# Optimization experiments

Measured on AMD Instinct MI355X. Metric: run time of the kernel, lower is better.

## Reference

```python
import jax, jax.numpy as jnp
import numpy as np

NQ, NT, NA = 10000, 50000, 50000
E_GR, E_LT, E_SIM, E_COMP, E_GEN = 50000, 50000, 80000, 100000, 50000
HID, NH, HC, DOT, NL = 512, 4, 128, 256, 2
NEG_SLOPE = 0.2  # PyG GATv2Conv default negative_slope


def _gatv2(x_src, x_dst, src, dst, Wl, bl, Wr, br, att, bias, n_dst):
    # GATv2: x_j = lin_l(x_src), x_i = lin_r(x_dst); e = att . leaky_relu(x_i + x_j)
    xl = (x_src @ Wl + bl).reshape(-1, NH, HC)   # [Ns,H,C]
    xr = (x_dst @ Wr + br).reshape(-1, NH, HC)   # [Nd,H,C]
    m = jax.nn.leaky_relu(xl[src] + xr[dst], NEG_SLOPE)      # [E,H,C]
    logits = jnp.einsum('ehc,hc->eh', m, att)                # [E,H]
    lmax = jax.lax.stop_gradient(jax.ops.segment_max(logits, dst, num_segments=n_dst))
    lmax = jnp.where(jnp.isfinite(lmax), lmax, 0.0)
    ex = jnp.exp(logits - lmax[dst])
    denom = jax.ops.segment_sum(ex, dst, num_segments=n_dst)
    alpha = ex / (denom[dst] + 1e-16)                        # softmax over incoming edges
    out = jax.ops.segment_sum(xl[src] * alpha[:, :, None], dst, num_segments=n_dst)
    return out.reshape(n_dst, NH * HC) + bias


def _layernorm(x, g, b):
    mu = x.mean(-1, keepdims=True)
    var = ((x - mu) ** 2).mean(-1, keepdims=True)
    return (x - mu) / jnp.sqrt(var + 1e-5) * g + b


def _forward(xq, xt, xa, answer_features,
             qp_W, qp_b, tp_W, tp_b, ap_W, ap_b,
             afp_W1, afp_b1, afp_W2, afp_b2,
             conv_Wl, conv_bl, conv_Wr, conv_br, conv_att, conv_bias,
             qh_W, qh_b, qh_g, qh_beta, rh_W, rh_b, rh_g, rh_beta, score_bias,
             ei_gr, ei_lt, ei_sim, ei_comp, ei_gen):
    hq = xq @ qp_W + qp_b
    ht = xt @ tp_W + tp_b
    ha = xa @ ap_W + ap_b
    # add_self_loops=True only for ('query','similar_to','query')
    loops = jnp.arange(NQ, dtype=ei_sim.dtype)
    sim_src = jnp.concatenate([ei_sim[0], loops])
    sim_dst = jnp.concatenate([ei_sim[1], loops])
    for l in range(NL):
        P = lambda r: (conv_Wl[l, r], conv_bl[l, r], conv_Wr[l, r], conv_br[l, r], conv_att[l, r], conv_bias[l, r])
        o_gr = _gatv2(hq, ht, ei_gr[0], ei_gr[1], *P(0), NT)          # query -> think
        o_rgr = _gatv2(ht, hq, ei_gr[1], ei_gr[0], *P(1), NQ)         # think -> query (rev)
        o_lt = _gatv2(ht, ha, ei_lt[0], ei_lt[1], *P(2), NA)          # think -> answer
        o_rlt = _gatv2(ha, ht, ei_lt[1], ei_lt[0], *P(3), NT)         # answer -> think (rev)
        o_sim = _gatv2(hq, hq, sim_src, sim_dst, *P(4), NQ)           # query -> query
        o_cmp = _gatv2(ht, ht, ei_comp[0], ei_comp[1], *P(5), NT)     # think -> think
        # HeteroConv aggr='mean' across relations per destination type, then relu
        hq = jax.nn.relu((o_rgr + o_sim) / 2.0)
        ht = jax.nn.relu((o_gr + o_rlt + o_cmp) / 3.0)
        ha = jax.nn.relu(o_lt)
    q_emb = hq[ei_gen[0]]
    a_emb = ha[ei_gen[1]]
    t_emb = ht[ei_gen[1]]  # faithful to source: think indexed with answer-side index
    af_emb = jax.nn.relu(answer_features @ afp_W1 + afp_b1) @ afp_W2 + afp_b2
    q = _layernorm(q_emb @ qh_W + qh_b, qh_g, qh_beta)
    r = _layernorm(jnp.concatenate([t_emb, a_emb, af_emb], -1) @ rh_W + rh_b, rh_g, rh_beta)
    return (q * r).sum(-1) / jnp.sqrt(jnp.float32(DOT)) + score_bias


def setup_inputs() -> dict:
    ks = jax.random.split(jax.random.key(0), 40)
    n = lambda j, shape, s=0.05: jax.random.normal(ks[j], shape, jnp.float32) * s
    ri = lambda j, shape, hi: jax.random.randint(ks[j], shape, 0, hi, jnp.int32)
    return dict(
        xq=n(0, (NQ, 384), 1.0), xt=n(1, (NT, 384), 1.0), xa=n(2, (NA, 384), 1.0),
        answer_features=n(3, (E_GEN, 6), 1.0),
        qp_W=n(4, (384, HID)), qp_b=n(5, (HID,)),
        tp_W=n(6, (384, HID)), tp_b=n(7, (HID,)),
        ap_W=n(8, (384, HID)), ap_b=n(9, (HID,)),
        afp_W1=n(10, (6, 64)), afp_b1=n(11, (64,)),
        afp_W2=n(12, (64, HID)), afp_b2=n(13, (HID,)),
        conv_Wl=n(14, (NL, 6, HID, HID)), conv_bl=n(15, (NL, 6, HID)),
        conv_Wr=n(16, (NL, 6, HID, HID)), conv_br=n(17, (NL, 6, HID)),
        conv_att=n(18, (NL, 6, NH, HC)), conv_bias=n(19, (NL, 6, HID)),
        qh_W=n(20, (HID, DOT)), qh_b=n(21, (DOT,)),
        qh_g=jnp.ones((DOT,), jnp.float32), qh_beta=jnp.zeros((DOT,), jnp.float32),
        rh_W=n(22, (HID * 3, DOT)), rh_b=n(23, (DOT,)),
        rh_g=jnp.ones((DOT,), jnp.float32), rh_beta=jnp.zeros((DOT,), jnp.float32),
        score_bias=jnp.zeros((1,), jnp.float32),
        ei_gr=jnp.stack([ri(24, (E_GR,), NQ), ri(25, (E_GR,), NT)]),
        ei_lt=jnp.stack([ri(26, (E_LT,), NT), ri(27, (E_LT,), NA)]),
        ei_sim=ri(28, (2, E_SIM), NQ),
        ei_comp=ri(29, (2, E_COMP), NT),
        ei_gen=jnp.stack([ri(30, (E_GEN,), NQ), ri(31, (E_GEN,), NA)]),
    )


def reference(xq, xt, xa, answer_features,
              qp_W, qp_b, tp_W, tp_b, ap_W, ap_b,
              afp_W1, afp_b1, afp_W2, afp_b2,
              conv_Wl, conv_bl, conv_Wr, conv_br, conv_att, conv_bias,
              qh_W, qh_b, qh_g, qh_beta, rh_W, rh_b, rh_g, rh_beta, score_bias,
              ei_gr, ei_lt, ei_sim, ei_comp, ei_gen):
    return _forward(xq, xt, xa, answer_features,
                    qp_W, qp_b, tp_W, tp_b, ap_W, ap_b,
                    afp_W1, afp_b1, afp_W2, afp_b2,
                    conv_Wl, conv_bl, conv_Wr, conv_br, conv_att, conv_bias,
                    qh_W, qh_b, qh_g, qh_beta, rh_W, rh_b, rh_g, rh_beta, score_bias,
                    ei_gr, ei_lt, ei_sim, ei_comp, ei_gen)
```

## Files before the change

### kernel.cpp

```cpp
#include <hip/hip_runtime.h>
#include <cstdio>
#include <type_traits>

#define NQ 10000
#define NT 50000
#define NA 50000
#define E_GR 50000
#define E_LT 50000
#define E_SIM 80000
#define E_COMP 100000
#define E_GEN 50000
#define NEG_SLOPE 0.2f

#define NDTOT 220000
#define NSTOT 220000
#define ETOT  390000
__device__ __constant__ const int c_degOff[7]  = {0, 50000, 60000, 110000, 120000, 170000, 220000};
__device__ __constant__ const int c_sOff[7]    = {0, 10000, 60000, 110000, 120000, 170000, 220000};
__device__ __constant__ const int c_eOff[7]    = {0, 50000, 100000, 150000, 240000, 340000, 390000};
__device__ __constant__ const int c_nb[6]      = {49, 10, 49, 10, 49, 49};
__device__ __constant__ const int c_nbOff[7]   = {0, 49, 59, 108, 118, 167, 216};
__device__ __constant__ const int c_snb[6]     = {10, 49, 49, 10, 49, 49};
__device__ __constant__ const int c_snbOff[7]  = {0, 10, 59, 108, 118, 167, 216};

typedef unsigned short bf16_t;
typedef unsigned int u32;
typedef __attribute__((ext_vector_type(8))) short short8v;
typedef __attribute__((ext_vector_type(4))) float f32x4;

__device__ __forceinline__ float bf2f(u32 bits) { return __uint_as_float(bits << 16); }
__device__ __forceinline__ u32 f2bf(float f) {
  u32 u = __float_as_uint(f);
  return (u + 0x7FFFu + ((u >> 16) & 1u)) >> 16;
}
__device__ __forceinline__ u32 pack2(float a, float b) { return f2bf(a) | (f2bf(b) << 16); }
__device__ __forceinline__ void unpack8(uint4 u, float* f) {
  f[0] = bf2f(u.x & 0xffffu); f[1] = bf2f(u.x >> 16);
  f[2] = bf2f(u.y & 0xffffu); f[3] = bf2f(u.y >> 16);
  f[4] = bf2f(u.z & 0xffffu); f[5] = bf2f(u.z >> 16);
  f[6] = bf2f(u.w & 0xffffu); f[7] = bf2f(u.w >> 16);
}

__device__ __forceinline__ void gload16(const void* g, void* l) {
  __builtin_amdgcn_global_load_lds(
      (const __attribute__((address_space(1))) void*)g,
      (__attribute__((address_space(3))) void*)l, 16, 0, 0);
}

template <typename CT>
__global__ __launch_bounds__(512, 4) void bgemm(
    const bf16_t* __restrict__ A0, const bf16_t* __restrict__ Bt0,
    const float* __restrict__ bias0, CT* __restrict__ C0,
    const int* __restrict__ ridx0, int N0, const int* __restrict__ Nc0,
    const bf16_t* __restrict__ A1, const bf16_t* __restrict__ Bt1,
    const float* __restrict__ bias1, CT* __restrict__ C1,
    const int* __restrict__ ridx1, int N1, const int* __restrict__ Nc1,
    int K, int M, int accumulate)
{
  __shared__ short lds[3][12288];
  const int z = blockIdx.z;
  const bf16_t* A   = z ? A1 : A0;
  const bf16_t* Bt  = z ? Bt1 : Bt0;
  const float* bias = z ? bias1 : bias0;
  CT* C             = z ? C1 : C0;
  const int* ridx   = z ? ridx1 : ridx0;
  const int* Nc     = z ? Nc1 : Nc0;
  int N             = z ? N1 : N0;
  if (Nc) N = *Nc;

  const int tid = threadIdx.x;
  const int ncol = gridDim.x;
  const int nband = (N + 127) >> 7;
  int lin = blockIdx.y * ncol + blockIdx.x;
  if (lin >= ncol * nband) return;

  int band, col;
  const int full = (nband >> 3) * 8 * ncol;
  if (lin < full) {
    int g = lin >> 3, x = lin & 7;
    band = x + 8 * (g / ncol);
    col  = g % ncol;
  } else {
    int r = lin - full;
    band = (nband & ~7) + r / ncol;
    col  = r % ncol;
  }
  const int bm = band * 128, bn = col * 256;

  const int lane = tid & 63;
  const int w = tid >> 6;
  const int wr = w >> 2, wc = w & 3;
  const int fr = lane & 15, fg = lane >> 4;

  const int kg = (((tid & 3) ^ ((tid >> 3) & 3)) << 3);
  const int rr = tid >> 2;
  int ra = min(bm + rr, N - 1);
  const bf16_t* gA0 = A + (size_t)(ridx ? ridx[ra] : ra) * K + kg;
  const bf16_t* gB0 = Bt + (size_t)(bn + rr) * K + kg;
  const bf16_t* gB1 = Bt + (size_t)(bn + 128 + rr) * K + kg;
  const int wb = w << 9;

  f32x4 acc[4][4];
#pragma unroll
  for (int i = 0; i < 4; ++i)
#pragma unroll
    for (int j = 0; j < 4; ++j) acc[i][j] = (f32x4){0.f, 0.f, 0.f, 0.f};

  auto stage = [&](int buf, int k0) {
    short* base = &lds[buf][0];
    gload16(gA0 + k0, base + wb);
    gload16(gB0 + k0, base + 4096 + wb);
    gload16(gB1 + k0, base + 8192 + wb);
  };

  const int nsteps = K >> 5;
  stage(0, 0);
  const int co = (fg ^ ((fr >> 1) & 3)) << 3;
  for (int s = 0; s < nsteps; ++s) {
    const int cur = s % 3;
    if (s + 1 < nsteps) {
      stage((s + 1) % 3, (s + 1) << 5);
      asm volatile("s_waitcnt vmcnt(3)" ::: "memory");
    } else {
      asm volatile("s_waitcnt vmcnt(0)" ::: "memory");
    }
    __builtin_amdgcn_s_barrier();
    asm volatile("" ::: "memory");
    const short* LA = &lds[cur][0];
    const short* LB = &lds[cur][4096];
    short8v b[4];
#pragma unroll
    for (int j = 0; j < 4; ++j) {
      int R = wc * 64 + j * 16 + fr;
      b[j] = *(const short8v*)&LB[R * 32 + co];
    }
#pragma unroll
    for (int i = 0; i < 4; ++i) {
      int R = wr * 64 + i * 16 + fr;
      short8v a = *(const short8v*)&LA[R * 32 + co];
#pragma unroll
      for (int j = 0; j < 4; ++j)
        acc[i][j] = __builtin_amdgcn_mfma_f32_16x16x32_bf16(b[j], a,
                                                            acc[i][j], 0, 0, 0);
    }
    asm volatile("" ::: "memory");
  }

  float4 bv[4];
#pragma unroll
  for (int j = 0; j < 4; ++j) {
    bv[j] = make_float4(0.f, 0.f, 0.f, 0.f);
    if (!accumulate && bias)
      bv[j] = *(const float4*)(bias + bn + wc * 64 + j * 16 + fg * 4);
  }
#pragma unroll
  for (int i = 0; i < 4; ++i) {
    const int n = bm + wr * 64 + i * 16 + fr;
    if (n >= N) continue;
#pragma unroll
    for (int j = 0; j < 4; ++j) {
      const int m0 = bn + wc * 64 + j * 16 + fg * 4;
      f32x4 v = acc[i][j];
      if constexpr (std::is_same<CT, float>::value) {
        float* p = C + (size_t)n * M + m0;
        if (accumulate) {
          float4 o = *(float4*)p;
          o.x += v[0]; o.y += v[1]; o.z += v[2]; o.w += v[3];
          *(float4*)p = o;
        } else {
          *(float4*)p = make_float4(v[0] + bv[j].x, v[1] + bv[j].y,
                                    v[2] + bv[j].z, v[3] + bv[j].w);
        }
      } else {
        uint2 o;
        o.x = pack2(v[0] + bv[j].x, v[1] + bv[j].y);
        o.y = pack2(v[2] + bv[j].z, v[3] + bv[j].w);
        *(uint2*)(C + (size_t)n * M + m0) = o;
      }
    }
  }
}

__device__ __forceinline__ void wT_tile(
    const float* __restrict__ W, bf16_t* __restrict__ Wt, int K, int M)
{
  __shared__ float sm[32][33];
  int mb = blockIdx.x * 32, kb = blockIdx.y * 32;
  int tx = threadIdx.x & 31, ty = threadIdx.x >> 5;
#pragma unroll
  for (int i = 0; i < 4; ++i)
    sm[ty + i * 8][tx] = W[(size_t)(kb + ty + i * 8) * M + mb + tx];
  __syncthreads();
#pragma unroll
  for (int i = 0; i < 4; ++i)
    Wt[(size_t)(mb + ty + i * 8) * K + kb + tx] = (bf16_t)f2bf(sm[tx][ty + i * 8]);
}

__global__ __launch_bounds__(256) void convert_wT(
    const float* __restrict__ W, bf16_t* __restrict__ Wt, int K, int M)
{
  wT_tile(W + (size_t)blockIdx.z * K * M, Wt + (size_t)blockIdx.z * K * M, K, M);
}
__global__ __launch_bounds__(256) void convert_wT24(
    const float* __restrict__ Wl, bf16_t* __restrict__ wl,
    const float* __restrict__ Wr, bf16_t* __restrict__ wr)
{
  int z = blockIdx.z;
  size_t o = (size_t)(z < 12 ? z : z - 12) * 512 * 512;
  if (z < 12) wT_tile(Wl + o, wl + o, 512, 512);
  else        wT_tile(Wr + o, wr + o, 512, 512);
}
__global__ __launch_bounds__(256) void convert_wT3(
    const float* __restrict__ W0, const float* __restrict__ W1,
    const float* __restrict__ W2, bf16_t* __restrict__ T0,
    bf16_t* __restrict__ T1, bf16_t* __restrict__ T2)
{
  int z = blockIdx.z;
  const float* W = z == 0 ? W0 : z == 1 ? W1 : W2;
  bf16_t* T = z == 0 ? T0 : z == 1 ? T1 : T2;
  wT_tile(W, T, 384, 512);
}
__global__ __launch_bounds__(256) void convert_wT4h(
    const float* __restrict__ qh, const float* __restrict__ rh,
    bf16_t* __restrict__ wqh, bf16_t* __restrict__ wrh)
{
  int z = blockIdx.z;
  if (z == 0) wT_tile(qh, wqh, 512, 256);
  else        wT_tile(rh + (size_t)(z - 1) * 512 * 256,
                      wrh + (size_t)(z - 1) * 256 * 512, 512, 256);
}

#define N4_XQ (NQ * 96)
#define N4_XT (NT * 96)
#define N4_XA (NA * 96)
__global__ __launch_bounds__(256) void cast3(
    const float* __restrict__ xq, const float* __restrict__ xt,
    const float* __restrict__ xa, bf16_t* __restrict__ xqb,
    bf16_t* __restrict__ xtb, bf16_t* __restrict__ xab)
{
  long g = (long)blockIdx.x * 256 + threadIdx.x;
  const float* in; bf16_t* out; long idx;
  if (g < N4_XQ)                { in = xq; out = xqb; idx = g; }
  else if (g < N4_XQ + N4_XT)   { in = xt; out = xtb; idx = g - N4_XQ; }
  else if (g < N4_XQ + N4_XT + N4_XA) { in = xa; out = xab; idx = g - N4_XQ - N4_XT; }
  else return;
  float4 v = ((const float4*)in)[idx];
  uint2 o;
  o.x = pack2(v.x, v.y);
  o.y = pack2(v.z, v.w);
  ((uint2*)out)[idx] = o;
}

__global__ __launch_bounds__(256) void combine_bias6(
    const float* __restrict__ cb, float* __restrict__ bcAll)
{
  int g = blockIdx.x * 256 + threadIdx.x;
  if (g >= 6 * 512) return;
  int row = g >> 9, j = g & 511;
  int l = row / 3, kind = row % 3;
  const float* b = cb + (size_t)l * 6 * 512;
  float v;
  if (kind == 0)      v = (b[0 * 512 + j] + b[3 * 512 + j] + b[5 * 512 + j]) / 3.f;
  else if (kind == 1) v = (b[1 * 512 + j] + b[4 * 512 + j]) * 0.5f;
  else                v = b[2 * 512 + j];
  bcAll[(size_t)row * 512 + j] = v;
}

__device__ __forceinline__ int find_rel6(int g, const int* off) {
  int r = 0;
#pragma unroll
  for (int k = 1; k < 6; ++k) r += (g >= off[k]);
  return r;
}

__global__ __launch_bounds__(256) void hist6(
    const int* __restrict__ d0, const int* __restrict__ d1,
    const int* __restrict__ d2, const int* __restrict__ d3,
    const int* __restrict__ d4, const int* __restrict__ d5,
    const int* __restrict__ s0p, const int* __restrict__ s1p,
    const int* __restrict__ s2p, const int* __restrict__ s3p,
    const int* __restrict__ s4p, const int* __restrict__ s5p,
    int* __restrict__ degAll, int* __restrict__ sdegAll, int* __restrict__ pos)
{
  int g = blockIdx.x * 256 + threadIdx.x;
  if (g >= ETOT) return;
  int r = find_rel6(g, c_eOff);
  int le = g - c_eOff[r];
  const int* dp = r == 0 ? d0 : r == 1 ? d1 : r == 2 ? d2 : r == 3 ? d3
                : r == 4 ? d4 : d5;
  const int* sp = r == 0 ? s0p : r == 1 ? s1p : r == 2 ? s2p : r == 3 ? s3p
                : r == 4 ? s4p : s5p;
  pos[g] = atomicAdd(&degAll[c_degOff[r] + dp[le]], 1);
  atomicAdd(&sdegAll[c_sOff[r] + sp[le]], 1);
}

template <int PRED, int SRC>
__global__ __launch_bounds__(256) void scan1_6(
    const int* __restrict__ in, int* __restrict__ out, int* __restrict__ bsum)
{
  __shared__ int sm[256];
  int b = blockIdx.x;
  const int* nbOff = SRC ? c_snbOff : c_nbOff;
  const int* dOff  = SRC ? c_sOff : c_degOff;
  int r = 0;
#pragma unroll
  for (int k = 1; k < 6; ++k) r += (b >= nbOff[k]);
  int lb = b - nbOff[r];
  int base0 = dOff[r], n = dOff[r + 1] - base0;
  int t = threadIdx.x;
  int base = lb * 1024 + t * 4;
  int v[4], sum = 0;
#pragma unroll
  for (int k = 0; k < 4; ++k) {
    int raw = (base + k < n) ? in[base0 + base + k] : 0;
    v[k] = PRED == 0 ? raw : PRED == 1 ? (raw >= 2 ? 1 : 0) : (raw >= 1 ? 1 : 0);
    sum += v[k];
  }
  sm[t] = sum;
  __syncthreads();
  for (int off = 1; off < 256; off <<= 1) {
    int x = (t >= off) ? sm[t - off] : 0;
    __syncthreads();
    sm[t] += x;
    __syncthreads();
  }
  int run = (t > 0) ? sm[t - 1] : 0;
  if (t == 255) bsum[r * 64 + lb] = sm[255];
#pragma unroll
  for (int k = 0; k < 4; ++k) {
    if (base + k < n) out[base0 + base + k] = run;
    run += v[k];
  }
}

template <int SRC>
__global__ __launch_bounds__(64) void scan2_6(
    int* __restrict__ bsum, int* __restrict__ total)
{
  __shared__ int sm[64];
  int r = blockIdx.x;
  int nb = SRC ? c_snb[r] : c_nb[r];
  int t = threadIdx.x;
  int v = (t < nb) ? bsum[r * 64 + t] : 0;
  sm[t] = v;
  __syncthreads();
  for (int off = 1; off < 64; off <<= 1) {
    int x = (t >= off) ? sm[t - off] : 0;
    __syncthreads();
    sm[t] += x;
    __syncthreads();
  }
  if (t < nb) bsum[r * 64 + t] = sm[t] - v;
  if (total && t == nb - 1) total[r] = sm[t];
}

template <int SRC>
__global__ __launch_bounds__(256) void scan3_6(
    int* __restrict__ out, const int* __restrict__ bsum)
{
  int g = blockIdx.x * 256 + threadIdx.x;
  if (g >= (SRC ? NSTOT : NDTOT)) return;
  const int* dOff = SRC ? c_sOff : c_degOff;
  int r = find_rel6(g, dOff);
  int ln = g - dOff[r];
  out[g] += bsum[r * 64 + (ln >> 10)];
}

__global__ __launch_bounds__(256) void scatter6(
    const int* __restrict__ d0, const int* __restrict__ d1,
    const int* __restrict__ d2, const int* __restrict__ d3,
    const int* __restrict__ d4, const int* __restrict__ d5,
    const int* __restrict__ s0p, const int* __restrict__ s1p,
    const int* __restrict__ s2p, const int* __restrict__ s3p,
    const int* __restrict__ s4p, const int* __restrict__ s5p,
    const int* __restrict__ startAll, const int* __restrict__ pos,
    const int* __restrict__ sposAll,
    int* __restrict__ eidxAll, int* __restrict__ srcCAll)
{
  int g = blockIdx.x * 256 + threadIdx.x;
  if (g >= ETOT) return;
  int r = find_rel6(g, c_eOff);
  int le = g - c_eOff[r];
  const int* dp = r == 0 ? d0 : r == 1 ? d1 : r == 2 ? d2 : r == 3 ? d3
                : r == 4 ? d4 : d5;
  const int* sp = r == 0 ? s0p : r == 1 ? s1p : r == 2 ? s2p : r == 3 ? s3p
                : r == 4 ? s4p : s5p;
  eidxAll[c_eOff[r] + startAll[c_degOff[r] + dp[le]] + pos[g]] = le;
  srcCAll[g] = sposAll[c_sOff[r] + sp[le]];
}

template <int SRC, int THR>
__global__ __launch_bounds__(256) void compact6(
    const int* __restrict__ degA, const int* __restrict__ cposA,
    int* __restrict__ cidxA)
{
  int g = blockIdx.x * 256 + threadIdx.x;
  if (g >= (SRC ? NSTOT : NDTOT)) return;
  if (degA[g] >= THR) {
    const int* dOff = SRC ? c_sOff : c_degOff;
    int r = find_rel6(g, dOff);
    cidxA[dOff[r] + cposA[g]] = g - dOff[r];
  }
}

__global__ __launch_bounds__(256) void gat_fused(
    const bf16_t* __restrict__ xl, const bf16_t* __restrict__ xr,
    const int* __restrict__ srcC, const int* __restrict__ start,
    const int* __restrict__ deg, const int* __restrict__ eidx,
    const int* __restrict__ cpos, const float* __restrict__ att,
    bf16_t* __restrict__ acc, int Nd, int accumulate,
    const float* __restrict__ bc, float inv_div)
{
  int d = blockIdx.x * 4 + (threadIdx.x >> 6);
  if (d >= Nd) return;
  int lane = threadIdx.x & 63;

  float acc8[8] = {0.f, 0.f, 0.f, 0.f, 0.f, 0.f, 0.f, 0.f};
  int n = deg[d], s0 = start[d];
  if (n == 1) {
    int s = srcC[eidx[s0]];
    unpack8(*(const uint4*)(xl + (size_t)s * 512 + lane * 8), acc8);
  } else if (n > 1) {
    float xrr[8];
    unpack8(*(const uint4*)(xr + (size_t)cpos[d] * 512 + lane * 8), xrr);
    float at[8];
    *(float4*)(at)     = *(const float4*)(att + lane * 8);
    *(float4*)(at + 4) = *(const float4*)(att + lane * 8 + 4);
    float den = 0.f;
    int sN = srcC[eidx[s0]];
    for (int i = 0; i < n; ++i) {
      int s = sN;
      if (i + 1 < n) sN = srcC[eidx[s0 + i + 1]];
      float f[8];
      unpack8(*(const uint4*)(xl + (size_t)s * 512 + lane * 8), f);
      float p = 0.f;
#pragma unroll
      for (int k = 0; k < 8; ++k) {
        float x = f[k] + xrr[k];
        p = fmaf(at[k], x >= 0.f ? x : NEG_SLOPE * x, p);
      }
#pragma unroll
      for (int m = 8; m >= 1; m >>= 1) p += __shfl_xor(p, m);
      float ex = __expf(p);
      den += ex;
#pragma unroll
      for (int k = 0; k < 8; ++k) acc8[k] = fmaf(ex, f[k], acc8[k]);
    }
    float inv = 1.f / (den + 1e-16f);
#pragma unroll
    for (int k = 0; k < 8; ++k) acc8[k] *= inv;
  }

  bf16_t* out = acc + (size_t)d * 512 + lane * 8;
  if (accumulate) {
    float old[8];
    unpack8(*(const uint4*)out, old);
#pragma unroll
    for (int k = 0; k < 8; ++k) acc8[k] += old[k];
  }
  if (bc) {
    float bcv[8];
    *(float4*)(bcv)     = *(const float4*)(bc + lane * 8);
    *(float4*)(bcv + 4) = *(const float4*)(bc + lane * 8 + 4);
#pragma unroll
    for (int k = 0; k < 8; ++k)
      acc8[k] = fmaxf(fmaf(acc8[k], inv_div, bcv[k]), 0.f);
  }
  uint4 s;
  s.x = pack2(acc8[0], acc8[1]); s.y = pack2(acc8[2], acc8[3]);
  s.z = pack2(acc8[4], acc8[5]); s.w = pack2(acc8[6], acc8[7]);
  *(uint4*)out = s;
}

__global__ __launch_bounds__(256) void af_hidden(
    const float* __restrict__ af, const float* __restrict__ W1,
    const float* __restrict__ b1, bf16_t* __restrict__ out, int n)
{
  int t = blockIdx.x * blockDim.x + threadIdx.x;
  if (t >= n * 64) return;
  int i = t >> 6, j = t & 63;
  const float* a = af + (size_t)i * 6;
  float s = b1[j];
#pragma unroll
  for (int k = 0; k < 6; ++k) s = fmaf(a[k], W1[k * 64 + j], s);
  out[t] = (bf16_t)f2bf(fmaxf(s, 0.f));
}

__global__ __launch_bounds__(256) void build_sim(
    const int* __restrict__ ei, int* __restrict__ ss, int* __restrict__ sd)
{
  int t = blockIdx.x * blockDim.x + threadIdx.x;
  if (t >= E_SIM + NQ) return;
  if (t < E_SIM) { ss[t] = ei[t]; sd[t] = ei[E_SIM + t]; }
  else           { ss[t] = t - E_SIM; sd[t] = t - E_SIM; }
}

__global__ __launch_bounds__(256) void head_final(
    const float* __restrict__ qpre, const float* __restrict__ rpre,
    const float* __restrict__ qg, const float* __restrict__ qb,
    const float* __restrict__ rg, const float* __restrict__ rb,
    const float* __restrict__ score_bias, float* __restrict__ out, int E)
{
  int e = blockIdx.x * 4 + (threadIdx.x >> 6);
  if (e >= E) return;
  int lane = threadIdx.x & 63;

  float4 q = *(const float4*)(qpre + (size_t)e * 256 + lane * 4);
  float s = q.x + q.y + q.z + q.w;
#pragma unroll
  for (int m = 32; m >= 1; m >>= 1) s += __shfl_xor(s, m);
  float mu = s * (1.f / 256.f);
  float dq0 = q.x - mu, dq1 = q.y - mu, dq2 = q.z - mu, dq3 = q.w - mu;
  float v = dq0 * dq0 + dq1 * dq1 + dq2 * dq2 + dq3 * dq3;
#pragma unroll
  for (int m = 32; m >= 1; m >>= 1) v += __shfl_xor(v, m);
  float rstd = rsqrtf(v * (1.f / 256.f) + 1e-5f);
  float4 g4 = *(const float4*)(qg + lane * 4);
  float4 b4 = *(const float4*)(qb + lane * 4);
  float qn0 = dq0 * rstd * g4.x + b4.x, qn1 = dq1 * rstd * g4.y + b4.y;
  float qn2 = dq2 * rstd * g4.z + b4.z, qn3 = dq3 * rstd * g4.w + b4.w;

  float4 r = *(const float4*)(rpre + (size_t)e * 256 + lane * 4);
  s = r.x + r.y + r.z + r.w;
#pragma unroll
  for (int m = 32; m >= 1; m >>= 1) s += __shfl_xor(s, m);
  mu = s * (1.f / 256.f);
  float dr0 = r.x - mu, dr1 = r.y - mu, dr2 = r.z - mu, dr3 = r.w - mu;
  v = dr0 * dr0 + dr1 * dr1 + dr2 * dr2 + dr3 * dr3;
#pragma unroll
  for (int m = 32; m >= 1; m >>= 1) v += __shfl_xor(v, m);
  rstd = rsqrtf(v * (1.f / 256.f) + 1e-5f);
  g4 = *(const float4*)(rg + lane * 4);
  b4 = *(const float4*)(rb + lane * 4);
  float rn0 = dr0 * rstd * g4.x + b4.x, rn1 = dr1 * rstd * g4.y + b4.y;
  float rn2 = dr2 * rstd * g4.z + b4.z, rn3 = dr3 * rstd * g4.w + b4.w;

  float d = qn0 * rn0 + qn1 * rn1 + qn2 * rn2 + qn3 * rn3;
#pragma unroll
  for (int m = 32; m >= 1; m >>= 1) d += __shfl_xor(d, m);
  if (lane == 0) out[e] = d * 0.0625f + score_bias[0];
}

extern "C" void kernel_launch(void* const* d_in, const int* in_sizes, int n_in,
                              void* d_out, int out_size, void* d_ws, size_t ws_size,
                              hipStream_t stream) {
  (void)in_sizes; (void)n_in; (void)out_size;
  const float* xq      = (const float*)d_in[0];
  const float* xt      = (const float*)d_in[1];
  const float* xa      = (const float*)d_in[2];
  const float* af      = (const float*)d_in[3];
  const float* qp_W    = (const float*)d_in[4];
  const float* qp_b    = (const float*)d_in[5];
  const float* tp_W    = (const float*)d_in[6];
  const float* tp_b    = (const float*)d_in[7];
  const float* ap_W    = (const float*)d_in[8];
  const float* ap_b    = (const float*)d_in[9];
  const float* afp_W1  = (const float*)d_in[10];
  const float* afp_b1  = (const float*)d_in[11];
  const float* afp_W2  = (const float*)d_in[12];
  const float* afp_b2  = (const float*)d_in[13];
  const float* conv_Wl = (const float*)d_in[14];
  const float* conv_bl = (const float*)d_in[15];
  const float* conv_Wr = (const float*)d_in[16];
  const float* conv_br = (const float*)d_in[17];
  const float* conv_att  = (const float*)d_in[18];
  const float* conv_bias = (const float*)d_in[19];
  const float* qh_W    = (const float*)d_in[20];
  const float* qh_b    = (const float*)d_in[21];
  const float* qh_g    = (const float*)d_in[22];
  const float* qh_beta = (const float*)d_in[23];
  const float* rh_W    = (const float*)d_in[24];
  const float* rh_b    = (const float*)d_in[25];
  const float* rh_g    = (const float*)d_in[26];
  const float* rh_beta = (const float*)d_in[27];
  const float* score_b = (const float*)d_in[28];
  const int* ei_gr   = (const int*)d_in[29];
  const int* ei_lt   = (const int*)d_in[30];
  const int* ei_sim  = (const int*)d_in[31];
  const int* ei_comp = (const int*)d_in[32];
  const int* ei_gen  = (const int*)d_in[33];

  char* base = (char*)d_ws;
  size_t off = 0;
  auto alloc = [&](size_t bytes) {
    void* p = base + off;
    off = (off + bytes + 255) & ~(size_t)255;
    return p;
  };
  bf16_t* hq   = (bf16_t*)alloc((size_t)NQ * 512 * 2);
  bf16_t* ht   = (bf16_t*)alloc((size_t)NT * 512 * 2);
  bf16_t* ha   = (bf16_t*)alloc((size_t)NA * 512 * 2);
  bf16_t* acct = (bf16_t*)alloc((size_t)NT * 512 * 2);
  bf16_t* accq = (bf16_t*)alloc((size_t)NQ * 512 * 2);
  bf16_t* xlb  = (bf16_t*)alloc((size_t)50000 * 512 * 2);
  bf16_t* xrb  = (bf16_t*)alloc((size_t)50000 * 512 * 2);
  int* simsrc  = (int*)alloc((size_t)(E_SIM + NQ) * 4);
  int* simdst  = (int*)alloc((size_t)(E_SIM + NQ) * 4);

  bf16_t* wqp  = (bf16_t*)alloc((size_t)512 * 384 * 2);
  bf16_t* wtp  = (bf16_t*)alloc((size_t)512 * 384 * 2);
  bf16_t* wap  = (bf16_t*)alloc((size_t)512 * 384 * 2);
  bf16_t* wl   = (bf16_t*)alloc((size_t)12 * 512 * 512 * 2);
  bf16_t* wr   = (bf16_t*)alloc((size_t)12 * 512 * 512 * 2);
  bf16_t* wafp2 = (bf16_t*)alloc((size_t)512 * 64 * 2);
  bf16_t* wqh  = (bf16_t*)alloc((size_t)256 * 512 * 2);
  bf16_t* wrh0 = (bf16_t*)alloc((size_t)256 * 512 * 2);
  bf16_t* wrh1 = (bf16_t*)alloc((size_t)256 * 512 * 2);
  bf16_t* wrh2 = (bf16_t*)alloc((size_t)256 * 512 * 2);
  float* bcAll = (float*)alloc(6 * 512 * 4);

  int* degAll   = (int*)alloc((size_t)NDTOT * 4);
  int* startAll = (int*)alloc((size_t)NDTOT * 4);
  int* cposAll  = (int*)alloc((size_t)NDTOT * 4);
  int* cidxAll  = (int*)alloc((size_t)NDTOT * 4);
  int* sdegAll  = (int*)alloc((size_t)NSTOT * 4);
  int* sposAll  = (int*)alloc((size_t)NSTOT * 4);
  int* sidxAll  = (int*)alloc((size_t)NSTOT * 4);
  int* eidxAll  = (int*)alloc((size_t)ETOT * 4);
  int* srcCAll  = (int*)alloc((size_t)ETOT * 4);
  int* posb     = (int*)alloc((size_t)ETOT * 4);
  int* bsum     = (int*)alloc(6 * 64 * 4);
  int* bsum2    = (int*)alloc(6 * 64 * 4);
  int* sbsum    = (int*)alloc(6 * 64 * 4);
  int* ccount   = (int*)alloc(6 * 4);
  int* scount   = (int*)alloc(6 * 4);
  if (off > ws_size) {
    fprintf(stderr, "kernel_launch: ws too small, need %zu have %zu\n", off, ws_size);
    return;
  }

  const int degOff[6] = {0, 50000, 60000, 110000, 120000, 170000};
  const int sOff[6]   = {0, 10000, 60000, 110000, 120000, 170000};
  const int eOff[6]   = {0, 50000, 100000, 150000, 240000, 340000};

  convert_wT24<<<dim3(16, 16, 24), 256, 0, stream>>>(conv_Wl, wl, conv_Wr, wr);
  convert_wT3<<<dim3(16, 12, 3), 256, 0, stream>>>(qp_W, tp_W, ap_W, wqp, wtp, wap);
  convert_wT4h<<<dim3(8, 16, 4), 256, 0, stream>>>(qh_W, rh_W, wqh, wrh0);
  convert_wT<<<dim3(16, 2, 1), 256, 0, stream>>>(afp_W2, wafp2, 64, 512);
  combine_bias6<<<(6 * 512 + 255) / 256, 256, 0, stream>>>(conv_bias, bcAll);

  build_sim<<<(E_SIM + NQ + 255) / 256, 256, 0, stream>>>(ei_sim, simsrc, simdst);
  const int* dsts[6]  = {ei_gr + E_GR, ei_gr, ei_lt, simdst,
                         ei_comp + E_COMP, ei_lt + E_LT};
  const int* srcsA[6] = {ei_gr, ei_gr + E_GR, ei_lt + E_LT, simsrc,
                         ei_comp, ei_lt};
  hipMemsetAsync(degAll, 0, (size_t)NDTOT * 4, stream);
  hipMemsetAsync(sdegAll, 0, (size_t)NSTOT * 4, stream);
  hist6<<<(ETOT + 255) / 256, 256, 0, stream>>>(
      dsts[0], dsts[1], dsts[2], dsts[3], dsts[4], dsts[5],
      srcsA[0], srcsA[1], srcsA[2], srcsA[3], srcsA[4], srcsA[5],
      degAll, sdegAll, posb);
  scan1_6<0, 0><<<216, 256, 0, stream>>>(degAll, startAll, bsum);
  scan1_6<1, 0><<<216, 256, 0, stream>>>(degAll, cposAll, bsum2);
  scan1_6<2, 1><<<216, 256, 0, stream>>>(sdegAll, sposAll, sbsum);
  scan2_6<0><<<6, 64, 0, stream>>>(bsum, nullptr);
  scan2_6<0><<<6, 64, 0, stream>>>(bsum2, ccount);
  scan2_6<1><<<6, 64, 0, stream>>>(sbsum, scount);
  scan3_6<0><<<(NDTOT + 255) / 256, 256, 0, stream>>>(startAll, bsum);
  scan3_6<0><<<(NDTOT + 255) / 256, 256, 0, stream>>>(cposAll, bsum2);
  scan3_6<1><<<(NSTOT + 255) / 256, 256, 0, stream>>>(sposAll, sbsum);
  scatter6<<<(ETOT + 255) / 256, 256, 0, stream>>>(
      dsts[0], dsts[1], dsts[2], dsts[3], dsts[4], dsts[5],
      srcsA[0], srcsA[1], srcsA[2], srcsA[3], srcsA[4], srcsA[5],
      startAll, posb, sposAll, eidxAll, srcCAll);
  compact6<0, 2><<<(NDTOT + 255) / 256, 256, 0, stream>>>(degAll, cposAll, cidxAll);
  compact6<1, 1><<<(NSTOT + 255) / 256, 256, 0, stream>>>(sdegAll, sposAll, sidxAll);

  auto gemm1 = [&](const bf16_t* A, const bf16_t* Bt, const float* bias, bf16_t* C,
                   int N_, int K_, int M_, const int* ridx = nullptr) {
    dim3 g(M_ / 256, (N_ + 127) / 128, 1);
    bgemm<bf16_t><<<g, 512, 0, stream>>>(A, Bt, bias, C, ridx, N_, nullptr,
                                         A, Bt, bias, C, ridx, N_, nullptr,
                                         K_, M_, 0);
  };
  auto gemmf1 = [&](const bf16_t* A, const bf16_t* Bt, const float* bias, float* C,
                    int N_, int K_, int M_, int acc_, const int* ridx = nullptr) {
    dim3 g(M_ / 256, (N_ + 127) / 128, 1);
    bgemm<float><<<g, 512, 0, stream>>>(A, Bt, bias, C, ridx, N_, nullptr,
                                        A, Bt, bias, C, ridx, N_, nullptr,
                                        K_, M_, acc_);
  };
  auto gemm2 = [&](const bf16_t* A0, const bf16_t* B0, const float* b0, bf16_t* C0, int N0_,
                   const bf16_t* A1, const bf16_t* B1, const float* b1, bf16_t* C1, int N1_,
                   int K_, int M_) {
    int nb0 = (N0_ + 127) / 128, nb1 = (N1_ + 127) / 128;
    dim3 g(M_ / 256, nb0 > nb1 ? nb0 : nb1, 2);
    bgemm<bf16_t><<<g, 512, 0, stream>>>(A0, B0, b0, C0, nullptr, N0_, nullptr,
                                         A1, B1, b1, C1, nullptr, N1_, nullptr,
                                         K_, M_, 0);
  };
  auto gemm2cc = [&](const bf16_t* A0, const bf16_t* B0, const float* b0, bf16_t* C0,
                     const int* sidx, int N0max, const int* Ns_,
                     const bf16_t* A1, const bf16_t* B1, const float* b1, bf16_t* C1,
                     const int* cidx, int N1max, const int* Ncnt) {
    int nb0 = (N0max + 127) / 128, nb1 = (N1max + 127) / 128;
    dim3 g(2, nb0 > nb1 ? nb0 : nb1, 2);
    bgemm<bf16_t><<<g, 512, 0, stream>>>(A0, B0, b0, C0, sidx, N0max, Ns_,
                                         A1, B1, b1, C1, cidx, N1max, Ncnt,
                                         512, 512, 0);
  };
  auto gemmf2 = [&](const bf16_t* A0, const bf16_t* B0, const float* b0, float* C0,
                    const int* r0, int N0_,
                    const bf16_t* A1, const bf16_t* B1, const float* b1, float* C1,
                    const int* r1, int N1_, int K_, int M_) {
    int nb0 = (N0_ + 127) / 128, nb1 = (N1_ + 127) / 128;
    dim3 g(M_ / 256, nb0 > nb1 ? nb0 : nb1, 2);
    bgemm<float><<<g, 512, 0, stream>>>(A0, B0, b0, C0, r0, N0_, nullptr,
                                        A1, B1, b1, C1, r1, N1_, nullptr,
                                        K_, M_, 0);
  };

  cast3<<<((long)(N4_XQ + N4_XT + N4_XA) + 255) / 256, 256, 0, stream>>>(
      xq, xt, xa, accq, xlb, xrb);
  gemm1(accq, wqp, qp_b, hq, NQ, 384, 512);
  gemm2(xlb, wtp, tp_b, ht, NT, xrb, wap, ap_b, ha, NA, 384, 512);

  const int NdArr[6] = {NT, NQ, NT, NQ, NT, NA};
  const int NsArr[6] = {NQ, NT, NA, NQ, NT, NT};
  bf16_t *hq_i = hq, *ht_i = ht, *hq_o = accq, *ht_o = acct;
  for (int l = 0; l < 2; ++l) {
    const float* bc_t = bcAll + (size_t)(l * 3 + 0) * 512;
    const float* bc_q = bcAll + (size_t)(l * 3 + 1) * 512;
    const float* bc_a = bcAll + (size_t)(l * 3 + 2) * 512;

    struct Rel { const bf16_t* xs; const bf16_t* xd; int po; bf16_t* acc;
                 int accum; const float* bc; float inv; };
    Rel rels[6] = {
      {hq_i, ht_i, 0, ht_o, 0, nullptr, 0.f},
      {ht_i, hq_i, 1, hq_o, 0, nullptr, 0.f},
      {ha,   ht_i, 3, ht_o, 1, nullptr, 0.f},
      {hq_i, hq_i, 4, hq_o, 1, bc_q, 0.5f},
      {ht_i, ht_i, 5, ht_o, 1, bc_t, 1.f / 3.f},
      {ht_i, ha,   2, ha,   0, bc_a, 1.f},
    };
    for (int r = 0; r < 6; ++r) {
      const Rel& R = rels[r];
      int Nd_ = NdArr[r];
      size_t po = (size_t)l * 6 + R.po;
      gemm2cc(R.xs, wl + po * 512 * 512, conv_bl + po * 512, xlb,
              sidxAll + sOff[r], NsArr[r], scount + r,
              R.xd, wr + po * 512 * 512, conv_br + po * 512, xrb,
              cidxAll + degOff[r], Nd_, ccount + r);
      int gb = (Nd_ + 3) / 4;
      gat_fused<<<gb, 256, 0, stream>>>(xlb, xrb, srcCAll + eOff[r],
                                        startAll + degOff[r], degAll + degOff[r],
                                        eidxAll + eOff[r], cposAll + degOff[r],
                                        conv_att + po * 512,
                                        R.acc, Nd_, R.accum, R.bc, R.inv);
    }
    bf16_t* t;
    t = hq_i; hq_i = hq_o; hq_o = t;
    t = ht_i; ht_i = ht_o; ht_o = t;
  }

  float* qpre = (float*)acct;
  float* rpre = (float*)xrb;
  bf16_t* afh = accq;
  const int* gsrc = ei_gen;
  const int* gdst = ei_gen + E_GEN;

  gemmf2(hq_i, wqh, qh_b, qpre, gsrc, E_GEN,
         ht_i, wrh0, rh_b, rpre, gdst, E_GEN, 512, 256);
  gemmf1(ha, wrh1, nullptr, rpre, E_GEN, 512, 256, 1, gdst);
  af_hidden<<<(E_GEN * 64 + 255) / 256, 256, 0, stream>>>(af, afp_W1, afp_b1,
                                                          afh, E_GEN);
  gemm1(afh, wafp2, afp_b2, xlb, E_GEN, 64, 512);
  gemmf1(xlb, wrh2, nullptr, rpre, E_GEN, 512, 256, 1);
  head_final<<<(E_GEN + 3) / 4, 256, 0, stream>>>(
      qpre, rpre, qh_g, qh_beta, rh_g, rh_beta, score_b, (float*)d_out, E_GEN);
}
```

Baseline: 1.251 ms.

## Fold answer-feature projection into head weights and gather head projections per node

The second answer-feature linear layer (64->512) is algebraically composed with the third slice of the readout head weight into a single 64->256 matrix plus a constant bias vector, both computed in a setup step. This removes a large 50000x64x512 GEMM and a 512-wide intermediate. Head projections for queries and think/answer nodes are now computed once per node (NQ/NT/NA rows) instead of per generated edge, and head_final gathers them by edge index. The trade-off is extra rounding from the bf16 folded weight and gathered random reads in the final kernel.

Result: faster. 1.207 ms (-3.5%).

```diff
diff --git a/kernel.cpp b/kernel.cpp
--- a/kernel.cpp
+++ b/kernel.cpp
@@ -230,6 +230,28 @@
                       wrh + (size_t)(z - 1) * 256 * 512, 512, 256);
 }
 
+__global__ __launch_bounds__(256) void cast_flat(
+    const float* __restrict__ in, bf16_t* __restrict__ out, int n4)
+{
+  int t = blockIdx.x * 256 + threadIdx.x;
+  if (t >= n4) return;
+  float4 v = ((const float4*)in)[t];
+  uint2 o;
+  o.x = pack2(v.x, v.y);
+  o.y = pack2(v.z, v.w);
+  ((uint2*)out)[t] = o;
+}
+
+__global__ __launch_bounds__(256) void fold_cvec(
+    const float* __restrict__ b2, const float* __restrict__ rh2,
+    float* __restrict__ cvec)
+{
+  int m = threadIdx.x;
+  float s = 0.f;
+  for (int k = 0; k < 512; ++k) s = fmaf(b2[k], rh2[(size_t)k * 256 + m], s);
+  cvec[m] = s;
+}
+
 #define N4_XQ (NQ * 96)
 #define N4_XT (NT * 96)
 #define N4_XA (NA * 96)
@@ -496,7 +518,9 @@
 }
 
 __global__ __launch_bounds__(256) void head_final(
-    const float* __restrict__ qpre, const float* __restrict__ rpre,
+    const float* __restrict__ qn, const float* __restrict__ rn,
+    const float* __restrict__ afr, const float* __restrict__ cvec,
+    const int* __restrict__ gsrc, const int* __restrict__ gdst,
     const float* __restrict__ qg, const float* __restrict__ qb,
     const float* __restrict__ rg, const float* __restrict__ rb,
     const float* __restrict__ score_bias, float* __restrict__ out, int E)
@@ -505,7 +529,7 @@
   if (e >= E) return;
   int lane = threadIdx.x & 63;
 
-  float4 q = *(const float4*)(qpre + (size_t)e * 256 + lane * 4);
+  float4 q = *(const float4*)(qn + (size_t)gsrc[e] * 256 + lane * 4);
   float s = q.x + q.y + q.z + q.w;
 #pragma unroll
   for (int m = 32; m >= 1; m >>= 1) s += __shfl_xor(s, m);
@@ -520,7 +544,14 @@
   float qn0 = dq0 * rstd * g4.x + b4.x, qn1 = dq1 * rstd * g4.y + b4.y;
   float qn2 = dq2 * rstd * g4.z + b4.z, qn3 = dq3 * rstd * g4.w + b4.w;
 
-  float4 r = *(const float4*)(rpre + (size_t)e * 256 + lane * 4);
+  float4 r0 = *(const float4*)(rn + (size_t)gdst[e] * 256 + lane * 4);
+  float4 r1 = *(const float4*)(afr + (size_t)e * 256 + lane * 4);
+  float4 cv = *(const float4*)(cvec + lane * 4);
+  float4 r;
+  r.x = r0.x + r1.x + cv.x;
+  r.y = r0.y + r1.y + cv.y;
+  r.z = r0.z + r1.z + cv.z;
+  r.w = r0.w + r1.w + cv.w;
   s = r.x + r.y + r.z + r.w;
 #pragma unroll
   for (int m = 32; m >= 1; m >>= 1) s += __shfl_xor(s, m);
@@ -602,12 +633,15 @@
   bf16_t* wap  = (bf16_t*)alloc((size_t)512 * 384 * 2);
   bf16_t* wl   = (bf16_t*)alloc((size_t)12 * 512 * 512 * 2);
   bf16_t* wr   = (bf16_t*)alloc((size_t)12 * 512 * 512 * 2);
-  bf16_t* wafp2 = (bf16_t*)alloc((size_t)512 * 64 * 2);
   bf16_t* wqh  = (bf16_t*)alloc((size_t)256 * 512 * 2);
   bf16_t* wrh0 = (bf16_t*)alloc((size_t)256 * 512 * 2);
   bf16_t* wrh1 = (bf16_t*)alloc((size_t)256 * 512 * 2);
   bf16_t* wrh2 = (bf16_t*)alloc((size_t)256 * 512 * 2);
   float* bcAll = (float*)alloc(6 * 512 * 4);
+  bf16_t* a2b    = (bf16_t*)alloc((size_t)64 * 512 * 2);
+  float*  wfoldF = (float*)alloc((size_t)64 * 256 * 4);
+  bf16_t* wfoldT = (bf16_t*)alloc((size_t)256 * 64 * 2);
+  float*  cvec   = (float*)alloc(256 * 4);
 
   int* degAll   = (int*)alloc((size_t)NDTOT * 4);
   int* startAll = (int*)alloc((size_t)NDTOT * 4);
@@ -632,39 +666,6 @@
   const int degOff[6] = {0, 50000, 60000, 110000, 120000, 170000};
   const int sOff[6]   = {0, 10000, 60000, 110000, 120000, 170000};
   const int eOff[6]   = {0, 50000, 100000, 150000, 240000, 340000};
-
-  convert_wT24<<<dim3(16, 16, 24), 256, 0, stream>>>(conv_Wl, wl, conv_Wr, wr);
-  convert_wT3<<<dim3(16, 12, 3), 256, 0, stream>>>(qp_W, tp_W, ap_W, wqp, wtp, wap);
-  convert_wT4h<<<dim3(8, 16, 4), 256, 0, stream>>>(qh_W, rh_W, wqh, wrh0);
-  convert_wT<<<dim3(16, 2, 1), 256, 0, stream>>>(afp_W2, wafp2, 64, 512);
-  combine_bias6<<<(6 * 512 + 255) / 256, 256, 0, stream>>>(conv_bias, bcAll);
-
-  build_sim<<<(E_SIM + NQ + 255) / 256, 256, 0, stream>>>(ei_sim, simsrc, simdst);
-  const int* dsts[6]  = {ei_gr + E_GR, ei_gr, ei_lt, simdst,
-                         ei_comp + E_COMP, ei_lt + E_LT};
-  const int* srcsA[6] = {ei_gr, ei_gr + E_GR, ei_lt + E_LT, simsrc,
-                         ei_comp, ei_lt};
-  hipMemsetAsync(degAll, 0, (size_t)NDTOT * 4, stream);
-  hipMemsetAsync(sdegAll, 0, (size_t)NSTOT * 4, stream);
-  hist6<<<(ETOT + 255) / 256, 256, 0, stream>>>(
-      dsts[0], dsts[1], dsts[2], dsts[3], dsts[4], dsts[5],
-      srcsA[0], srcsA[1], srcsA[2], srcsA[3], srcsA[4], srcsA[5],
-      degAll, sdegAll, posb);
-  scan1_6<0, 0><<<216, 256, 0, stream>>>(degAll, startAll, bsum);
-  scan1_6<1, 0><<<216, 256, 0, stream>>>(degAll, cposAll, bsum2);
-  scan1_6<2, 1><<<216, 256, 0, stream>>>(sdegAll, sposAll, sbsum);
-  scan2_6<0><<<6, 64, 0, stream>>>(bsum, nullptr);
-  scan2_6<0><<<6, 64, 0, stream>>>(bsum2, ccount);
-  scan2_6<1><<<6, 64, 0, stream>>>(sbsum, scount);
-  scan3_6<0><<<(NDTOT + 255) / 256, 256, 0, stream>>>(startAll, bsum);
-  scan3_6<0><<<(NDTOT + 255) / 256, 256, 0, stream>>>(cposAll, bsum2);
-  scan3_6<1><<<(NSTOT + 255) / 256, 256, 0, stream>>>(sposAll, sbsum);
-  scatter6<<<(ETOT + 255) / 256, 256, 0, stream>>>(
-      dsts[0], dsts[1], dsts[2], dsts[3], dsts[4], dsts[5],
-      srcsA[0], srcsA[1], srcsA[2], srcsA[3], srcsA[4], srcsA[5],
-      startAll, posb, sposAll, eidxAll, srcCAll);
-  compact6<0, 2><<<(NDTOT + 255) / 256, 256, 0, stream>>>(degAll, cposAll, cidxAll);
-  compact6<1, 1><<<(NSTOT + 255) / 256, 256, 0, stream>>>(sdegAll, sposAll, sidxAll);
 
   auto gemm1 = [&](const bf16_t* A, const bf16_t* Bt, const float* bias, bf16_t* C,
                    int N_, int K_, int M_, const int* ridx = nullptr) {
@@ -699,16 +700,51 @@
                                          A1, B1, b1, C1, cidx, N1max, Ncnt,
                                          512, 512, 0);
   };
-  auto gemmf2 = [&](const bf16_t* A0, const bf16_t* B0, const float* b0, float* C0,
-                    const int* r0, int N0_,
-                    const bf16_t* A1, const bf16_t* B1, const float* b1, float* C1,
-                    const int* r1, int N1_, int K_, int M_) {
+  auto gemmf2 = [&](const bf16_t* A0, const bf16_t* B0, const float* b0, float* C0, int N0_,
+                    const bf16_t* A1, const bf16_t* B1, const float* b1, float* C1, int N1_,
+                    int K_, int M_) {
     int nb0 = (N0_ + 127) / 128, nb1 = (N1_ + 127) / 128;
     dim3 g(M_ / 256, nb0 > nb1 ? nb0 : nb1, 2);
-    bgemm<float><<<g, 512, 0, stream>>>(A0, B0, b0, C0, r0, N0_, nullptr,
-                                        A1, B1, b1, C1, r1, N1_, nullptr,
+    bgemm<float><<<g, 512, 0, stream>>>(A0, B0, b0, C0, nullptr, N0_, nullptr,
+                                        A1, B1, b1, C1, nullptr, N1_, nullptr,
                                         K_, M_, 0);
   };
+
+  convert_wT24<<<dim3(16, 16, 24), 256, 0, stream>>>(conv_Wl, wl, conv_Wr, wr);
+  convert_wT3<<<dim3(16, 12, 3), 256, 0, stream>>>(qp_W, tp_W, ap_W, wqp, wtp, wap);
+  convert_wT4h<<<dim3(8, 16, 4), 256, 0, stream>>>(qh_W, rh_W, wqh, wrh0);
+  combine_bias6<<<(6 * 512 + 255) / 256, 256, 0, stream>>>(conv_bias, bcAll);
+  cast_flat<<<(64 * 512 / 4 + 255) / 256, 256, 0, stream>>>(afp_W2, a2b, 64 * 512 / 4);
+  gemmf1(a2b, wrh2, nullptr, wfoldF, 64, 512, 256, 0);
+  convert_wT<<<dim3(8, 2, 1), 256, 0, stream>>>(wfoldF, wfoldT, 64, 256);
+  fold_cvec<<<1, 256, 0, stream>>>(afp_b2, rh_W + 1024 * 256, cvec);
+
+  build_sim<<<(E_SIM + NQ + 255) / 256, 256, 0, stream>>>(ei_sim, simsrc, simdst);
+  const int* dsts[6]  = {ei_gr + E_GR, ei_gr, ei_lt, simdst,
+                         ei_comp + E_COMP, ei_lt + E_LT};
+  const int* srcsA[6] = {ei_gr, ei_gr + E_GR, ei_lt + E_LT, simsrc,
+                         ei_comp, ei_lt};
+  hipMemsetAsync(degAll, 0, (size_t)NDTOT * 4, stream);
+  hipMemsetAsync(sdegAll, 0, (size_t)NSTOT * 4, stream);
+  hist6<<<(ETOT + 255) / 256, 256, 0, stream>>>(
+      dsts[0], dsts[1], dsts[2], dsts[3], dsts[4], dsts[5],
+      srcsA[0], srcsA[1], srcsA[2], srcsA[3], srcsA[4], srcsA[5],
+      degAll, sdegAll, posb);
+  scan1_6<0, 0><<<216, 256, 0, stream>>>(degAll, startAll, bsum);
+  scan1_6<1, 0><<<216, 256, 0, stream>>>(degAll, cposAll, bsum2);
+  scan1_6<2, 1><<<216, 256, 0, stream>>>(sdegAll, sposAll, sbsum);
+  scan2_6<0><<<6, 64, 0, stream>>>(bsum, nullptr);
+  scan2_6<0><<<6, 64, 0, stream>>>(bsum2, ccount);
+  scan2_6<1><<<6, 64, 0, stream>>>(sbsum, scount);
+  scan3_6<0><<<(NDTOT + 255) / 256, 256, 0, stream>>>(startAll, bsum);
+  scan3_6<0><<<(NDTOT + 255) / 256, 256, 0, stream>>>(cposAll, bsum2);
+  scan3_6<1><<<(NSTOT + 255) / 256, 256, 0, stream>>>(sposAll, sbsum);
+  scatter6<<<(ETOT + 255) / 256, 256, 0, stream>>>(
+      dsts[0], dsts[1], dsts[2], dsts[3], dsts[4], dsts[5],
+      srcsA[0], srcsA[1], srcsA[2], srcsA[3], srcsA[4], srcsA[5],
+      startAll, posb, sposAll, eidxAll, srcCAll);
+  compact6<0, 2><<<(NDTOT + 255) / 256, 256, 0, stream>>>(degAll, cposAll, cidxAll);
+  compact6<1, 1><<<(NSTOT + 255) / 256, 256, 0, stream>>>(sdegAll, sposAll, sidxAll);
 
   cast3<<<((long)(N4_XQ + N4_XT + N4_XA) + 255) / 256, 256, 0, stream>>>(
       xq, xt, xa, accq, xlb, xrb);
@@ -753,19 +789,19 @@
     t = ht_i; ht_i = ht_o; ht_o = t;
   }
 
-  float* qpre = (float*)acct;
-  float* rpre = (float*)xrb;
-  bf16_t* afh = accq;
+  float* qn  = (float*)accq;
+  float* rn  = (float*)acct;
+  float* afr = (float*)xrb;
+  bf16_t* afh = xlb;
   const int* gsrc = ei_gen;
   const int* gdst = ei_gen + E_GEN;
 
-  gemmf2(hq_i, wqh, qh_b, qpre, gsrc, E_GEN,
-         ht_i, wrh0, rh_b, rpre, gdst, E_GEN, 512, 256);
-  gemmf1(ha, wrh1, nullptr, rpre, E_GEN, 512, 256, 1, gdst);
+  gemmf2(hq_i, wqh, qh_b, qn, NQ, ht_i, wrh0, rh_b, rn, NT, 512, 256);
+  gemmf1(ha, wrh1, nullptr, rn, NA, 512, 256, 1);
   af_hidden<<<(E_GEN * 64 + 255) / 256, 256, 0, stream>>>(af, afp_W1, afp_b1,
                                                           afh, E_GEN);
-  gemm1(afh, wafp2, afp_b2, xlb, E_GEN, 64, 512);
-  gemmf1(xlb, wrh2, nullptr, rpre, E_GEN, 512, 256, 1);
+  gemmf1(afh, wfoldT, nullptr, afr, E_GEN, 64, 256, 0);
   head_final<<<(E_GEN + 3) / 4, 256, 0, stream>>>(
-      qpre, rpre, qh_g, qh_beta, rh_g, rh_beta, score_b, (float*)d_out, E_GEN);
-}
+      qn, rn, afr, cvec, gsrc, gdst,
+      qh_g, qh_beta, rh_g, rh_beta, score_b, (float*)d_out, E_GEN);
+}
```
